# Kernel tuning notes

Measured on AMD Instinct MI355X. Metric: run time of the kernel, lower is better.

Reference implementation:

```python
import jax, jax.numpy as jnp
import numpy as np

IOU_THR = 0.5
SCORE_THR = 0.5
MAX_DET = 100
B, N, C = 16, 25200, 80


def setup_inputs() -> dict:
    key = jax.random.key(0)
    k1, k2, k3 = jax.random.split(key, 3)
    return {
        "boxes_xywh": jax.random.uniform(k1, (B, N, 4), dtype=jnp.float32),
        "objectness": jax.random.uniform(k2, (B, N, 1), dtype=jnp.float32),
        "class_prob": jax.random.uniform(k3, (B, N, C), dtype=jnp.float32),
    }


def _xywh_to_corners(b):
    x, y, w, h = jnp.split(b, 4, axis=-1)
    return jnp.concatenate([x - w / 2, y - h / 2, x + w / 2, y + h / 2], axis=-1)


def _broadcast_iou(box, boxes):
    # box [4], boxes [N,4] in x1,y1,x2,y2
    lt = jnp.maximum(box[:2], boxes[:, :2])
    rb = jnp.minimum(box[2:], boxes[:, 2:])
    wh = jnp.clip(rb - lt, 0.0)
    inter = wh[:, 0] * wh[:, 1]
    a1 = (box[2] - box[0]) * (box[3] - box[1])
    a2 = (boxes[:, 2] - boxes[:, 0]) * (boxes[:, 3] - boxes[:, 1])
    return inter / (a1 + a2 - inter + 1e-9)


def _nms_single(cand):
    # cand: [N, 4+1+C] rows = (x1,y1,x2,y2, score, class_probs...)
    n, d = cand.shape
    scores = cand[:, 4]
    active0 = scores >= SCORE_THR

    def body(i, state):
        active, out, count = state
        masked = jnp.where(active, scores, -jnp.inf)
        best = jnp.argmax(masked)
        valid = jnp.any(active)
        best_box = cand[best]
        out = out.at[i].set(jnp.where(valid, best_box, out[i]))
        count = count + valid.astype(jnp.int32)
        iou = _broadcast_iou(best_box[:4], cand[:, :4])
        keep = active & (iou <= IOU_THR)
        keep = keep.at[best].set(False)
        active = jnp.where(valid, keep, active)
        return active, out, count

    out0 = jnp.zeros((MAX_DET, d), cand.dtype)
    _, out, count = jax.lax.fori_loop(0, MAX_DET, body, (active0, out0, jnp.int32(0)))
    return out, count


def reference(boxes_xywh, objectness, class_prob):
    corners = _xywh_to_corners(boxes_xywh)  # [B,N,4]
    combined = jnp.concatenate([corners, objectness, class_prob], axis=-1)  # [B,N,5+C]
    final_result, count = jax.vmap(_nms_single)(combined)  # [B,MAX_DET,5+C], [B]
    nms_boxes = final_result[..., 0:4]
    nms_scores = final_result[..., 4:5]
    nms_classes = final_result[..., 5:]
    valid_count = count.astype(jnp.int32)[:, None]  # [B,1]
    return nms_boxes, nms_scores, nms_classes, valid_count
```

## Files before the change

### kernel.cpp

```cpp
#include <hip/hip_runtime.h>

#define NBOX    25200
#define NQ4     6300
#define NBATCH  16
#define NCLS    80
#define MAXDET  100
#define NBUCKET 1024
#define CAP     13824
#define SCORE_THR 0.5f
#define IOU_THR   0.5f
#define NGROUP  16
#define LAZY_BKT 896

__device__ __forceinline__ void mk_corners(float x, float y, float w, float h,
                                           float& x1, float& y1, float& x2, float& y2) {
#pragma clang fp contract(off)
    float hw = w * 0.5f;
    float hh = h * 0.5f;
    x1 = x - hw; y1 = y - hh; x2 = x + hw; y2 = y + hh;
}

__device__ __forceinline__ float areaf(float x1, float y1, float x2, float y2) {
#pragma clang fp contract(off)
    return (x2 - x1) * (y2 - y1);
}

__device__ __forceinline__ bool iou_gt(float kx1, float ky1, float kx2, float ky2, float ka,
                                       float cx1, float cy1, float cx2, float cy2, float ca) {
#pragma clang fp contract(off)
    float lx = fmaxf(kx1, cx1);
    float ly = fmaxf(ky1, cy1);
    float rx = fminf(kx2, cx2);
    float ry = fminf(ky2, cy2);
    float w  = fmaxf(rx - lx, 0.0f);
    float h  = fmaxf(ry - ly, 0.0f);
    float inter = w * h;
    float denom = ka + ca - inter + 1e-9f;
    return (inter / denom) > IOU_THR;
}

__device__ __forceinline__ float readlane_f(float v, int j) {
    return __uint_as_float((unsigned)__builtin_amdgcn_readlane((int)__float_as_uint(v), j));
}

__device__ __forceinline__ unsigned score_key(float s) {
    return __float_as_uint(s) - 0x3F000000u;
}

__global__ __launch_bounds__(1024)
void nms_kernel(const float* __restrict__ boxes_xywh,
                const float* __restrict__ objectness,
                const float* __restrict__ class_prob,
                float* __restrict__ out) {
    __shared__ unsigned s_hist[NBUCKET];
    __shared__ unsigned s_start[NBUCKET];
    __shared__ unsigned s_a[CAP];
    __shared__ unsigned s_b[CAP];
    __shared__ float4   s_kbox[MAXDET];
    __shared__ unsigned s_kept_idx[MAXDET];
    __shared__ unsigned s_wsum[16];
    __shared__ unsigned s_woff[16];
    __shared__ int      s_count;

    const int b = blockIdx.x;
    const int t = threadIdx.x;
    const int w = t >> 6;
    const int l = t & 63;
    const float* obj = objectness + (size_t)b * NBOX;
    const float* bx  = boxes_xywh + (size_t)b * NBOX * 4;

    float4 r[7];
#pragma unroll
    for (int i = 0; i < 7; ++i) {
        int n4 = t + (i << 10);
        if (n4 < NQ4) r[i] = *(const float4*)(obj + n4 * 4);
    }

    s_hist[t] = 0u;
    __syncthreads();
#pragma unroll
    for (int i = 0; i < 7; ++i) {
        int n4 = t + (i << 10);
        if (n4 < NQ4) {
            float sv[4] = {r[i].x, r[i].y, r[i].z, r[i].w};
#pragma unroll
            for (int u = 0; u < 4; ++u) {
                if (sv[u] >= SCORE_THR) {
                    unsigned bkt = score_key(sv[u]) >> 13;
                    if (bkt > 1023u) bkt = 1023u;
                    atomicAdd(&s_hist[bkt], 1u);
                }
            }
        }
    }
    __syncthreads();

    {
        unsigned f = s_hist[1023 - t];
        unsigned v = f;
#pragma unroll
        for (int off = 1; off < 64; off <<= 1) {
            unsigned u = (unsigned)__shfl_up((int)v, off);
            if (l >= off) v += u;
        }
        if (l == 63) s_wsum[w] = v;
        __syncthreads();
        if (t < 64) {
            unsigned x = (t < 16) ? s_wsum[t] : 0u;
            unsigned y = x;
#pragma unroll
            for (int off = 1; off < 16; off <<= 1) {
                unsigned u = (unsigned)__shfl_up((int)y, off);
                if (t >= off) y += u;
            }
            if (t < 16) s_woff[t] = y - x;
        }
        __syncthreads();
        s_start[1023 - t] = v - f + s_woff[w];
    }
    if (t == 0) s_count = 0;
    __syncthreads();

#pragma unroll
    for (int i = 0; i < 7; ++i) {
        int n4 = t + (i << 10);
        if (n4 < NQ4) {
            float sv[4] = {r[i].x, r[i].y, r[i].z, r[i].w};
#pragma unroll
            for (int u = 0; u < 4; ++u) {
                if (sv[u] >= SCORE_THR) {
                    unsigned ekey = score_key(sv[u]);
                    unsigned bkt  = ekey >> 13;
                    if (bkt > 1023u) bkt = 1023u;
                    if (bkt >= LAZY_BKT) {
                        int n = n4 * 4 + u;
                        unsigned pos = atomicAdd(&s_start[bkt], 1u);
                        if (pos < CAP)
                            s_a[pos] = ((ekey & 0x1FFFu) << 18) | (0x3FFFFu - (unsigned)n);
                    }
                }
            }
        }
    }
    __syncthreads();

    auto sort_bucket = [&](int bkt) {
        unsigned h = s_hist[bkt];
        if (h == 0u) return;
        unsigned end = s_start[bkt];
        unsigned hi  = (end > CAP) ? CAP : end;
        unsigned lo  = (end >= h) ? end - h : 0u;
        if (lo > hi) lo = hi;
        unsigned sz = hi - lo;
        if (sz == 0u) return;
        if (sz <= 64u) {
            unsigned v = (l < (int)sz) ? s_a[lo + (unsigned)l] : 0u;
            int rank = 0;
            for (unsigned j = 0; j < sz; ++j)
                rank += ((unsigned)__shfl((int)v, (int)j) > v) ? 1 : 0;
            if (l < (int)sz) s_b[lo + (unsigned)rank] = v;
        } else {
            for (unsigned bb = 0; bb < sz; bb += 64u) {
                bool valid = bb + (unsigned)l < sz;
                unsigned v = valid ? s_a[lo + bb + (unsigned)l] : 0u;
                int rank = 0;
                for (unsigned j = 0; j < sz; ++j)
                    rank += (s_a[lo + j] > v) ? 1 : 0;
                if (valid) s_b[lo + (unsigned)rank] = v;
            }
        }
    };

    for (int bkt = (1023 - 63) + w; bkt <= 1023; bkt += 16) sort_bucket(bkt);
    __syncthreads();

    int count = 0;
    int nscat = 2;
    for (int g = 0; g < NGROUP; ++g) {
        const int BH = 1023 - (g << 6);
        const int BL = BH - 63;

        if (g >= nscat) {
            for (int n4 = t; n4 < NQ4; n4 += 1024) {
                float4 s4 = *(const float4*)(obj + n4 * 4);
                float sv[4] = {s4.x, s4.y, s4.z, s4.w};
#pragma unroll
                for (int u = 0; u < 4; ++u) {
                    if (sv[u] >= SCORE_THR) {
                        unsigned ekey = score_key(sv[u]);
                        unsigned bkt  = ekey >> 13;
                        if (bkt > 1023u) bkt = 1023u;
                        if (bkt < LAZY_BKT) {
                            int n = n4 * 4 + u;
                            unsigned pos = atomicAdd(&s_start[bkt], 1u);
                            if (pos < CAP)
                                s_a[pos] = ((ekey & 0x1FFFu) << 18) | (0x3FFFFu - (unsigned)n);
                        }
                    }
                }
            }
            __syncthreads();
            nscat = NGROUP;
            for (int bkt = BL + w; bkt <= BH; bkt += 16) sort_bucket(bkt);
            __syncthreads();
        }

        if (w == 0) {
            unsigned glo = (g == 0) ? 0u : s_start[BH + 1];
            unsigned ghi = s_start[BL];
            if (glo > CAP) glo = CAP;
            if (ghi > CAP) ghi = CAP;

            if (glo < ghi && count < MAXDET) {
                unsigned i0, i1, i2, i3;
                float4 q0, q1, q2, q3;
                auto loadc = [&](unsigned cb, unsigned& ix, float4& q) {
                    ix = 0u; q = make_float4(0.f, 0.f, 0.f, 0.f);
                    unsigned p0 = cb + (unsigned)l;
                    if (p0 < ghi) {
                        unsigned p = s_b[p0];
                        ix = 0x3FFFFu - (p & 0x3FFFFu);
                        q = *(const float4*)(bx + (size_t)ix * 4);
                    }
                };
                loadc(glo,        i0, q0);
                loadc(glo + 64u,  i1, q1);
                loadc(glo + 128u, i2, q2);
                loadc(glo + 192u, i3, q3);

                for (unsigned base = glo; base < ghi && count < MAXDET; base += 64u) {
                    unsigned cidx = i0; float4 cq = q0;
                    i0 = i1; q0 = q1;
                    i1 = i2; q1 = q2;
                    i2 = i3; q2 = q3;
                    loadc(base + 256u, i3, q3);

                    int m = (int)(ghi - base); if (m > 64) m = 64;
                    float cx1, cy1, cx2, cy2;
                    mk_corners(cq.x, cq.y, cq.z, cq.w, cx1, cy1, cx2, cy2);
                    float ca = areaf(cx1, cy1, cx2, cy2);

                    bool sup = (l >= m);
                    int k = 0;
                    for (; k + 4 <= count; k += 4) {
                        float4 kb0 = s_kbox[k],     kb1 = s_kbox[k + 1];
                        float4 kb2 = s_kbox[k + 2], kb3 = s_kbox[k + 3];
                        sup = sup | iou_gt(kb0.x, kb0.y, kb0.z, kb0.w,
                                           areaf(kb0.x, kb0.y, kb0.z, kb0.w), cx1, cy1, cx2, cy2, ca);
                        sup = sup | iou_gt(kb1.x, kb1.y, kb1.z, kb1.w,
                                           areaf(kb1.x, kb1.y, kb1.z, kb1.w), cx1, cy1, cx2, cy2, ca);
                        sup = sup | iou_gt(kb2.x, kb2.y, kb2.z, kb2.w,
                                           areaf(kb2.x, kb2.y, kb2.z, kb2.w), cx1, cy1, cx2, cy2, ca);
                        sup = sup | iou_gt(kb3.x, kb3.y, kb3.z, kb3.w,
                                           areaf(kb3.x, kb3.y, kb3.z, kb3.w), cx1, cy1, cx2, cy2, ca);
                    }
                    for (; k < count; ++k) {
                        float4 kb = s_kbox[k];
                        sup = sup | iou_gt(kb.x, kb.y, kb.z, kb.w,
                                           areaf(kb.x, kb.y, kb.z, kb.w), cx1, cy1, cx2, cy2, ca);
                    }
                    unsigned long long act = __ballot(!sup);

                    unsigned long long accmask = 0ull;
                    const int cbase = count;
                    while (act != 0ull && count < MAXDET) {
                        int j = (int)__builtin_ctzll(act);
                        accmask |= 1ull << j;
                        float bx1 = readlane_f(cx1, j), by1 = readlane_f(cy1, j);
                        float bx2 = readlane_f(cx2, j), by2 = readlane_f(cy2, j);
                        float bar = readlane_f(ca, j);
                        bool su = iou_gt(bx1, by1, bx2, by2, bar, cx1, cy1, cx2, cy2, ca);
                        ++count;
                        act &= ~(1ull << j);
                        act &= ~__ballot(su);
                    }

                    if (accmask & (1ull << l)) {
                        int slot = cbase + (int)__popcll(accmask & ((1ull << l) - 1ull));
                        s_kbox[slot] = make_float4(cx1, cy1, cx2, cy2);
                        s_kept_idx[slot] = cidx;
                        float* ob = out + ((size_t)b * MAXDET + slot) * 4;
                        ob[0] = cx1; ob[1] = cy1; ob[2] = cx2; ob[3] = cy2;
                        out[NBATCH * MAXDET * 4 + b * MAXDET + slot] = obj[cidx];
                    }
                    __asm__ volatile("s_waitcnt lgkmcnt(0)" ::: "memory");
                }
            }
            if (l == 0) s_count = count;
        } else if (g + 1 < NGROUP && g + 1 < nscat) {
            const int BH2 = BH - 64, BL2 = BH2 - 63;
            for (int bkt = BL2 + (w - 1); bkt <= BH2; bkt += 15) sort_bucket(bkt);
        }
        __syncthreads();
        if (s_count >= MAXDET) break;
    }

    const int cf = s_count;
    for (int e = t; e < MAXDET * 4; e += 1024) {
        if ((e >> 2) >= cf) out[(size_t)b * MAXDET * 4 + e] = 0.0f;
    }
    for (int i = t; i < MAXDET; i += 1024) {
        if (i >= cf) out[NBATCH * MAXDET * 4 + b * MAXDET + i] = 0.0f;
    }
    const float* cp = class_prob + (size_t)b * NBOX * NCLS;
    float* oc = out + NBATCH * MAXDET * 5 + (size_t)b * MAXDET * NCLS;
    for (int e = t; e < cf * NCLS; e += 1024) {
        int i = e / NCLS;
        int c = e - i * NCLS;
        oc[e] = cp[(size_t)s_kept_idx[i] * NCLS + c];
    }
    for (int e = t + cf * NCLS; e < MAXDET * NCLS; e += 1024) oc[e] = 0.0f;
    if (t == 0)
        out[NBATCH * MAXDET * 5 + NBATCH * MAXDET * NCLS + b] = (float)cf;
}

extern "C" void kernel_launch(void* const* d_in, const int* in_sizes, int n_in,
                              void* d_out, int out_size, void* d_ws, size_t ws_size,
                              hipStream_t stream) {
    const float* boxes = (const float*)d_in[0];
    const float* objn  = (const float*)d_in[1];
    const float* clsp  = (const float*)d_in[2];
    float* out = (float*)d_out;
    nms_kernel<<<dim3(NBATCH), dim3(1024), 0, stream>>>(boxes, objn, clsp, out);
}
```

Measured before the change: 198.7 us.

## Sort all buckets eagerly and run NMS over 1024-candidate superblocks using all waves

Drops the lazy two-phase scatter and per-group bucket sort, and instead scatters and sorts every bucket up front. NMS then works on 1024-candidate superblocks. All 16 waves load candidates and test them in parallel against the already-kept boxes, while wave 0 resolves one 64-lane sub-chunk at a time and the other waves incrementally update their suppression masks. This spreads the suppression work across the whole block instead of serializing it on one wave, at the cost of sorting buckets that may never be needed and adding many block-wide barriers per superblock.

Measured after the change: 272.5 us. 1.37x slower.

```diff
diff --git a/kernel.cpp b/kernel.cpp
--- a/kernel.cpp
+++ b/kernel.cpp
@@ -9,8 +9,8 @@
 #define CAP     13824
 #define SCORE_THR 0.5f
 #define IOU_THR   0.5f
-#define NGROUP  16
-#define LAZY_BKT 896
+#define SUPER   1024
+#define NSUB    16
 
 __device__ __forceinline__ void mk_corners(float x, float y, float w, float h,
                                            float& x1, float& y1, float& x2, float& y2) {
@@ -56,10 +56,14 @@
     __shared__ unsigned s_start[NBUCKET];
     __shared__ unsigned s_a[CAP];
     __shared__ unsigned s_b[CAP];
+    __shared__ float4   s_cc[SUPER];
+    __shared__ float    s_ca[SUPER];
+    __shared__ unsigned long long s_mask[NSUB];
     __shared__ float4   s_kbox[MAXDET];
     __shared__ unsigned s_kept_idx[MAXDET];
     __shared__ unsigned s_wsum[16];
     __shared__ unsigned s_woff[16];
+    __shared__ int      s_cnt2[2];
     __shared__ int      s_count;
 
     const int b = blockIdx.x;
@@ -132,12 +136,10 @@
                     unsigned ekey = score_key(sv[u]);
                     unsigned bkt  = ekey >> 13;
                     if (bkt > 1023u) bkt = 1023u;
-                    if (bkt >= LAZY_BKT) {
-                        int n = n4 * 4 + u;
-                        unsigned pos = atomicAdd(&s_start[bkt], 1u);
-                        if (pos < CAP)
-                            s_a[pos] = ((ekey & 0x1FFFu) << 18) | (0x3FFFFu - (unsigned)n);
-                    }
+                    int n = n4 * 4 + u;
+                    unsigned pos = atomicAdd(&s_start[bkt], 1u);
+                    if (pos < CAP)
+                        s_a[pos] = ((ekey & 0x1FFFu) << 18) | (0x3FFFFu - (unsigned)n);
                 }
             }
         }
@@ -171,129 +173,125 @@
         }
     };
 
-    for (int bkt = (1023 - 63) + w; bkt <= 1023; bkt += 16) sort_bucket(bkt);
-    __syncthreads();
+    for (int bkt = w; bkt < NBUCKET; bkt += 16) sort_bucket(bkt);
+    __syncthreads();
+
+    unsigned total = s_start[0];
+    if (total > CAP) total = CAP;
 
     int count = 0;
-    int nscat = 2;
-    for (int g = 0; g < NGROUP; ++g) {
-        const int BH = 1023 - (g << 6);
-        const int BL = BH - 63;
-
-        if (g >= nscat) {
-            for (int n4 = t; n4 < NQ4; n4 += 1024) {
-                float4 s4 = *(const float4*)(obj + n4 * 4);
-                float sv[4] = {s4.x, s4.y, s4.z, s4.w};
-#pragma unroll
-                for (int u = 0; u < 4; ++u) {
-                    if (sv[u] >= SCORE_THR) {
-                        unsigned ekey = score_key(sv[u]);
-                        unsigned bkt  = ekey >> 13;
-                        if (bkt > 1023u) bkt = 1023u;
-                        if (bkt < LAZY_BKT) {
-                            int n = n4 * 4 + u;
-                            unsigned pos = atomicAdd(&s_start[bkt], 1u);
-                            if (pos < CAP)
-                                s_a[pos] = ((ekey & 0x1FFFu) << 18) | (0x3FFFFu - (unsigned)n);
-                        }
+    for (unsigned base = 0; base < total; base += SUPER) {
+        __syncthreads();
+        int count0 = s_count;
+        if (count0 >= MAXDET) break;
+
+        unsigned pos = base + (unsigned)t;
+        bool valid = pos < total;
+        float cx1 = 0.f, cy1 = 0.f, cx2 = 0.f, cy2 = 0.f, ca = 0.f;
+        if (valid) {
+            unsigned pk = s_b[pos];
+            unsigned ci = 0x3FFFFu - (pk & 0x3FFFFu);
+            float4 q = *(const float4*)(bx + (size_t)ci * 4);
+            mk_corners(q.x, q.y, q.z, q.w, cx1, cy1, cx2, cy2);
+            ca = areaf(cx1, cy1, cx2, cy2);
+        }
+        s_cc[t] = make_float4(cx1, cy1, cx2, cy2);
+        s_ca[t] = ca;
+        bool sup = !valid;
+        {
+            int k = 0;
+            for (; k + 4 <= count0; k += 4) {
+                float4 kb0 = s_kbox[k],     kb1 = s_kbox[k + 1];
+                float4 kb2 = s_kbox[k + 2], kb3 = s_kbox[k + 3];
+                sup = sup | iou_gt(kb0.x, kb0.y, kb0.z, kb0.w,
+                                   areaf(kb0.x, kb0.y, kb0.z, kb0.w), cx1, cy1, cx2, cy2, ca);
+                sup = sup | iou_gt(kb1.x, kb1.y, kb1.z, kb1.w,
+                                   areaf(kb1.x, kb1.y, kb1.z, kb1.w), cx1, cy1, cx2, cy2, ca);
+                sup = sup | iou_gt(kb2.x, kb2.y, kb2.z, kb2.w,
+                                   areaf(kb2.x, kb2.y, kb2.z, kb2.w), cx1, cy1, cx2, cy2, ca);
+                sup = sup | iou_gt(kb3.x, kb3.y, kb3.z, kb3.w,
+                                   areaf(kb3.x, kb3.y, kb3.z, kb3.w), cx1, cy1, cx2, cy2, ca);
+            }
+            for (; k < count0; ++k) {
+                float4 kb = s_kbox[k];
+                sup = sup | iou_gt(kb.x, kb.y, kb.z, kb.w,
+                                   areaf(kb.x, kb.y, kb.z, kb.w), cx1, cy1, cx2, cy2, ca);
+            }
+        }
+        {
+            unsigned long long m = __ballot(sup);
+            if (l == 0) s_mask[w] = m;
+        }
+        if (t == 0) s_cnt2[0] = count0;
+
+        int myprev = count0;
+        int cA = count0, cB = count0;
+
+        for (int sub = 0; sub < NSUB; ++sub) {
+            __syncthreads();
+            int ccur = s_cnt2[sub & 1];
+            if (ccur >= MAXDET) break;
+
+            if (w == 0) {
+                const int boff = (sub << 6) + l;
+                float4 cc = s_cc[boff];
+                float  ca2 = s_ca[boff];
+                unsigned long long mm = s_mask[sub];
+                bool sup2 = ((mm >> l) & 1ull) != 0ull;
+                for (int kk = cA; kk < cB; ++kk) {
+                    float4 kb = s_kbox[kk];
+                    sup2 = sup2 | iou_gt(kb.x, kb.y, kb.z, kb.w,
+                                         areaf(kb.x, kb.y, kb.z, kb.w),
+                                         cc.x, cc.y, cc.z, cc.w, ca2);
+                }
+                unsigned long long act = __ballot(!sup2);
+
+                unsigned long long accmask = 0ull;
+                const int cbase = count;
+                while (act != 0ull && count < MAXDET) {
+                    int j = (int)__builtin_ctzll(act);
+                    accmask |= 1ull << j;
+                    float bx1 = readlane_f(cc.x, j), by1 = readlane_f(cc.y, j);
+                    float bx2 = readlane_f(cc.z, j), by2 = readlane_f(cc.w, j);
+                    float bar = readlane_f(ca2, j);
+                    bool su = iou_gt(bx1, by1, bx2, by2, bar,
+                                     cc.x, cc.y, cc.z, cc.w, ca2);
+                    ++count;
+                    act &= ~(1ull << j);
+                    act &= ~__ballot(su);
+                }
+
+                if (accmask & (1ull << l)) {
+                    int slot = cbase + (int)__popcll(accmask & ((1ull << l) - 1ull));
+                    s_kbox[slot] = cc;
+                    unsigned pk2 = s_b[base + (unsigned)boff];
+                    unsigned ci  = 0x3FFFFu - (pk2 & 0x3FFFFu);
+                    s_kept_idx[slot] = ci;
+                    float* ob = out + ((size_t)b * MAXDET + slot) * 4;
+                    ob[0] = cc.x; ob[1] = cc.y; ob[2] = cc.z; ob[3] = cc.w;
+                    out[NBATCH * MAXDET * 4 + b * MAXDET + slot] = obj[ci];
+                }
+                cA = cB; cB = count;
+                if (l == 0) {
+                    s_count = count;
+                    s_cnt2[(sub + 1) & 1] = count;
+                }
+            } else if (w > sub) {
+                if (ccur > myprev) {
+                    for (int kk = myprev; kk < ccur; ++kk) {
+                        float4 kb = s_kbox[kk];
+                        sup = sup | iou_gt(kb.x, kb.y, kb.z, kb.w,
+                                           areaf(kb.x, kb.y, kb.z, kb.w),
+                                           cx1, cy1, cx2, cy2, ca);
                     }
-                }
-            }
-            __syncthreads();
-            nscat = NGROUP;
-            for (int bkt = BL + w; bkt <= BH; bkt += 16) sort_bucket(bkt);
-            __syncthreads();
-        }
-
-        if (w == 0) {
-            unsigned glo = (g == 0) ? 0u : s_start[BH + 1];
-            unsigned ghi = s_start[BL];
-            if (glo > CAP) glo = CAP;
-            if (ghi > CAP) ghi = CAP;
-
-            if (glo < ghi && count < MAXDET) {
-                unsigned i0, i1, i2, i3;
-                float4 q0, q1, q2, q3;
-                auto loadc = [&](unsigned cb, unsigned& ix, float4& q) {
-                    ix = 0u; q = make_float4(0.f, 0.f, 0.f, 0.f);
-                    unsigned p0 = cb + (unsigned)l;
-                    if (p0 < ghi) {
-                        unsigned p = s_b[p0];
-                        ix = 0x3FFFFu - (p & 0x3FFFFu);
-                        q = *(const float4*)(bx + (size_t)ix * 4);
-                    }
-                };
-                loadc(glo,        i0, q0);
-                loadc(glo + 64u,  i1, q1);
-                loadc(glo + 128u, i2, q2);
-                loadc(glo + 192u, i3, q3);
-
-                for (unsigned base = glo; base < ghi && count < MAXDET; base += 64u) {
-                    unsigned cidx = i0; float4 cq = q0;
-                    i0 = i1; q0 = q1;
-                    i1 = i2; q1 = q2;
-                    i2 = i3; q2 = q3;
-                    loadc(base + 256u, i3, q3);
-
-                    int m = (int)(ghi - base); if (m > 64) m = 64;
-                    float cx1, cy1, cx2, cy2;
-                    mk_corners(cq.x, cq.y, cq.z, cq.w, cx1, cy1, cx2, cy2);
-                    float ca = areaf(cx1, cy1, cx2, cy2);
-
-                    bool sup = (l >= m);
-                    int k = 0;
-                    for (; k + 4 <= count; k += 4) {
-                        float4 kb0 = s_kbox[k],     kb1 = s_kbox[k + 1];
-                        float4 kb2 = s_kbox[k + 2], kb3 = s_kbox[k + 3];
-                        sup = sup | iou_gt(kb0.x, kb0.y, kb0.z, kb0.w,
-                                           areaf(kb0.x, kb0.y, kb0.z, kb0.w), cx1, cy1, cx2, cy2, ca);
-                        sup = sup | iou_gt(kb1.x, kb1.y, kb1.z, kb1.w,
-                                           areaf(kb1.x, kb1.y, kb1.z, kb1.w), cx1, cy1, cx2, cy2, ca);
-                        sup = sup | iou_gt(kb2.x, kb2.y, kb2.z, kb2.w,
-                                           areaf(kb2.x, kb2.y, kb2.z, kb2.w), cx1, cy1, cx2, cy2, ca);
-                        sup = sup | iou_gt(kb3.x, kb3.y, kb3.z, kb3.w,
-                                           areaf(kb3.x, kb3.y, kb3.z, kb3.w), cx1, cy1, cx2, cy2, ca);
-                    }
-                    for (; k < count; ++k) {
-                        float4 kb = s_kbox[k];
-                        sup = sup | iou_gt(kb.x, kb.y, kb.z, kb.w,
-                                           areaf(kb.x, kb.y, kb.z, kb.w), cx1, cy1, cx2, cy2, ca);
-                    }
-                    unsigned long long act = __ballot(!sup);
-
-                    unsigned long long accmask = 0ull;
-                    const int cbase = count;
-                    while (act != 0ull && count < MAXDET) {
-                        int j = (int)__builtin_ctzll(act);
-                        accmask |= 1ull << j;
-                        float bx1 = readlane_f(cx1, j), by1 = readlane_f(cy1, j);
-                        float bx2 = readlane_f(cx2, j), by2 = readlane_f(cy2, j);
-                        float bar = readlane_f(ca, j);
-                        bool su = iou_gt(bx1, by1, bx2, by2, bar, cx1, cy1, cx2, cy2, ca);
-                        ++count;
-                        act &= ~(1ull << j);
-                        act &= ~__ballot(su);
-                    }
-
-                    if (accmask & (1ull << l)) {
-                        int slot = cbase + (int)__popcll(accmask & ((1ull << l) - 1ull));
-                        s_kbox[slot] = make_float4(cx1, cy1, cx2, cy2);
-                        s_kept_idx[slot] = cidx;
-                        float* ob = out + ((size_t)b * MAXDET + slot) * 4;
-                        ob[0] = cx1; ob[1] = cy1; ob[2] = cx2; ob[3] = cy2;
-                        out[NBATCH * MAXDET * 4 + b * MAXDET + slot] = obj[cidx];
-                    }
-                    __asm__ volatile("s_waitcnt lgkmcnt(0)" ::: "memory");
-                }
-            }
-            if (l == 0) s_count = count;
-        } else if (g + 1 < NGROUP && g + 1 < nscat) {
-            const int BH2 = BH - 64, BL2 = BH2 - 63;
-            for (int bkt = BL2 + (w - 1); bkt <= BH2; bkt += 15) sort_bucket(bkt);
-        }
-        __syncthreads();
-        if (s_count >= MAXDET) break;
-    }
+                    myprev = ccur;
+                    unsigned long long m2 = __ballot(sup);
+                    if (l == 0) s_mask[w] = m2;
+                }
+            }
+        }
+    }
+    __syncthreads();
 
     const int cf = s_count;
     for (int e = t; e < MAXDET * 4; e += 1024) {
```
